# Kernel optimization log

Hardware: AMD Instinct MI355X
Metric: run time of the kernel (lower is better)

The kernel has to match this reference:

```python
import jax, jax.numpy as jnp
import numpy as np

AUDIO_DIM = 1280
FR = 0.15   # freq_mask_ratio
TR = 0.2    # time_mask_ratio
NT = 2      # num_t
NF = 2      # num_f


def setup_inputs() -> dict:
    key = jax.random.key(0)
    k = jax.random.split(key, 6)
    B, T, D = 32, 2048, 1536
    X = jax.random.normal(k[0], (B, T, D), dtype=jnp.float32)
    lengths = jax.random.randint(k[1], (B,), 0, 2048).astype(jnp.int64)
    u_t = jax.random.uniform(k[2], (NT, B), dtype=jnp.float32)
    u_t0 = jax.random.uniform(k[3], (NT, B), dtype=jnp.float32)
    u_f = jax.random.uniform(k[4], (NF, B), dtype=jnp.float32)
    u_f0 = jax.random.uniform(k[5], (NF, B), dtype=jnp.float32)
    return {"X": X, "lengths": lengths, "u_t": u_t, "u_t0": u_t0,
            "u_f": u_f, "u_f0": u_f0}


def reference(X, lengths, u_t, u_t0, u_f, u_f0):
    B, T, D = X.shape
    A = AUDIO_DIM
    V = X[..., : D - A]          # video part, untouched
    Aud = X[..., D - A :]        # audio part, gets masked

    # ---- time masking (per sample, NT spans) ----
    len_i = lengths.astype(jnp.int32)                      # [B]
    max_t = jnp.floor(len_i.astype(jnp.float32) * TR)      # int(Ti*tr), [B]
    # t ~ randint(0, max_t+1): floor(u*(max_t+1))
    t = jnp.floor(u_t * (max_t[None, :] + 1.0)).astype(jnp.int32)   # [NT,B]
    rem = len_i[None, :] - t                                        # Ti - t
    # t0 = 0 if Ti-t<=0 else randint(0, Ti-t+1)
    t0 = jnp.where(rem <= 0, 0,
                   jnp.floor(u_t0 * (rem.astype(jnp.float32) + 1.0)).astype(jnp.int32))
    tt = jnp.arange(T, dtype=jnp.int32)[None, None, :]              # [1,1,T]
    tmask = jnp.any((tt >= t0[:, :, None]) & (tt < (t0 + t)[:, :, None]), axis=0)  # [B,T]

    # ---- frequency masking (per sample, NF spans) ----
    max_f = int(A * FR)
    f = jnp.floor(u_f * (max_f + 1.0)).astype(jnp.int32)            # [NF,B]
    f0_max = jnp.clip(A - f, 0, None)
    f0 = jnp.floor(u_f0 * (f0_max.astype(jnp.float32) + 1.0)).astype(jnp.int32)
    ff = jnp.arange(A, dtype=jnp.int32)[None, None, :]              # [1,1,A]
    fmask = jnp.any((ff >= f0[:, :, None]) & (ff < (f0 + f)[:, :, None]), axis=0)  # [B,A]

    keep = jnp.logical_not(tmask[:, :, None] | fmask[:, None, :]).astype(X.dtype)  # [B,T,A]
    return jnp.concatenate([V, Aud * keep], axis=-1)
```

## Files before the change

### kernel.cpp

```cpp
#include <hip/hip_runtime.h>

#define AUDIO_DIM_ 1280
#define B_ 32
#define T_ 2048
#define D_ 1536
#define V_ (D_ - AUDIO_DIM_)

__global__ void precompute_bounds(const int* __restrict__ lengths,
                                  const float* __restrict__ u_t,
                                  const float* __restrict__ u_t0,
                                  const float* __restrict__ u_f,
                                  const float* __restrict__ u_f0,
                                  int* __restrict__ bounds) {
    int b = threadIdx.x;
    if (b >= B_) return;
    int len = lengths[b];
    float max_t = floorf((float)len * 0.2f);
    int o[8];
    #pragma unroll
    for (int j = 0; j < 2; ++j) {
        int t   = (int)floorf(u_t[j * B_ + b] * (max_t + 1.0f));
        int rem = len - t;
        int t0  = (rem <= 0) ? 0 : (int)floorf(u_t0[j * B_ + b] * ((float)rem + 1.0f));
        o[2 * j]     = t0;
        o[2 * j + 1] = t0 + t;
    }
    #pragma unroll
    for (int j = 0; j < 2; ++j) {
        int f     = (int)floorf(u_f[j * B_ + b] * 193.0f);
        int f0max = AUDIO_DIM_ - f;
        if (f0max < 0) f0max = 0;
        int f0    = (int)floorf(u_f0[j * B_ + b] * ((float)f0max + 1.0f));
        o[4 + 2 * j] = f0;
        o[5 + 2 * j] = f0 + f;
    }
    int4* dst = (int4*)(bounds + b * 8);
    dst[0] = make_int4(o[0], o[1], o[2], o[3]);
    dst[1] = make_int4(o[4], o[5], o[6], o[7]);
}

__device__ __forceinline__ bool in_iv(int v, int lo, int hi) {
    return (v >= lo) && (v < hi);
}

__global__ __launch_bounds__(256) void specaug_kernel(const float4* __restrict__ X,
                                                      float4* __restrict__ out,
                                                      const int4* __restrict__ bounds) {
    constexpr int ND4  = D_ / 4;
    constexpr int NV4  = V_ / 4;
    constexpr int NTD4 = T_ * ND4;
    constexpr int N4   = B_ * NTD4;

    int stride = gridDim.x * blockDim.x;
    for (int idx = blockIdx.x * blockDim.x + threadIdx.x; idx < N4; idx += stride) {
        int b  = idx / NTD4;
        int r  = idx - b * NTD4;
        int t  = r / ND4;
        int d4 = r - t * ND4;

        float4 x = X[idx];

        if (d4 >= NV4) {
            int4 tb = bounds[2 * b];
            bool tm = in_iv(t, tb.x, tb.y) || in_iv(t, tb.z, tb.w);
            if (tm) {
                x = make_float4(0.f, 0.f, 0.f, 0.f);
            } else {
                int4 fb = bounds[2 * b + 1];
                int ff = (d4 - NV4) * 4;
                if (in_iv(ff + 0, fb.x, fb.y) || in_iv(ff + 0, fb.z, fb.w)) x.x = 0.f;
                if (in_iv(ff + 1, fb.x, fb.y) || in_iv(ff + 1, fb.z, fb.w)) x.y = 0.f;
                if (in_iv(ff + 2, fb.x, fb.y) || in_iv(ff + 2, fb.z, fb.w)) x.z = 0.f;
                if (in_iv(ff + 3, fb.x, fb.y) || in_iv(ff + 3, fb.z, fb.w)) x.w = 0.f;
            }
        }
        out[idx] = x;
    }
}

extern "C" void kernel_launch(void* const* d_in, const int* in_sizes, int n_in,
                              void* d_out, int out_size, void* d_ws, size_t ws_size,
                              hipStream_t stream) {
    const float* X       = (const float*)d_in[0];
    const int*   lengths = (const int*)  d_in[1];
    const float* u_t     = (const float*)d_in[2];
    const float* u_t0    = (const float*)d_in[3];
    const float* u_f     = (const float*)d_in[4];
    const float* u_f0    = (const float*)d_in[5];
    float*       out     = (float*)d_out;
    int*         bounds  = (int*)d_ws;

    precompute_bounds<<<1, 64, 0, stream>>>(lengths, u_t, u_t0, u_f, u_f0, bounds);

    specaug_kernel<<<12288, 256, 0, stream>>>((const float4*)X, (float4*)out,
                                              (const int4*)bounds);
}
```

Before: 643.0 us.

## Fuse bounds computation into a row-tiled kernel with nontemporal access and masked-row skipping

Drops the separate bounds-precompute launch; each block now derives its sample's time and frequency spans directly from the inputs. The grid becomes 2D (row tile × batch) with 384 threads covering one row of float4s, which removes the per-element div/mod of the grid-stride loop. The frequency mask is built once per thread as a float4 multiplier. Loads for time-masked audio rows are skipped, and loads and stores are nontemporal. Every block redundantly reads the small per-sample inputs. Multiplying by the mask differs from the reference only for non-finite inputs (NaN or Inf times 0 gives NaN, not 0), which random normal data never produces.

```diff
diff --git a/kernel.cpp b/kernel.cpp
--- a/kernel.cpp
+++ b/kernel.cpp
@@ -5,93 +5,95 @@
 #define T_ 2048
 #define D_ 1536
 #define V_ (D_ - AUDIO_DIM_)
+#define ND4_ (D_ / 4)
+#define NV4_ (V_ / 4)
+#define ROWS_ 8
 
-__global__ void precompute_bounds(const int* __restrict__ lengths,
-                                  const float* __restrict__ u_t,
-                                  const float* __restrict__ u_t0,
-                                  const float* __restrict__ u_f,
-                                  const float* __restrict__ u_f0,
-                                  int* __restrict__ bounds) {
-    int b = threadIdx.x;
-    if (b >= B_) return;
-    int len = lengths[b];
-    float max_t = floorf((float)len * 0.2f);
-    int o[8];
-    #pragma unroll
-    for (int j = 0; j < 2; ++j) {
-        int t   = (int)floorf(u_t[j * B_ + b] * (max_t + 1.0f));
-        int rem = len - t;
-        int t0  = (rem <= 0) ? 0 : (int)floorf(u_t0[j * B_ + b] * ((float)rem + 1.0f));
-        o[2 * j]     = t0;
-        o[2 * j + 1] = t0 + t;
-    }
-    #pragma unroll
-    for (int j = 0; j < 2; ++j) {
-        int f     = (int)floorf(u_f[j * B_ + b] * 193.0f);
-        int f0max = AUDIO_DIM_ - f;
-        if (f0max < 0) f0max = 0;
-        int f0    = (int)floorf(u_f0[j * B_ + b] * ((float)f0max + 1.0f));
-        o[4 + 2 * j] = f0;
-        o[5 + 2 * j] = f0 + f;
-    }
-    int4* dst = (int4*)(bounds + b * 8);
-    dst[0] = make_int4(o[0], o[1], o[2], o[3]);
-    dst[1] = make_int4(o[4], o[5], o[6], o[7]);
-}
+typedef float f4 __attribute__((ext_vector_type(4)));
 
 __device__ __forceinline__ bool in_iv(int v, int lo, int hi) {
     return (v >= lo) && (v < hi);
 }
 
-__global__ __launch_bounds__(256) void specaug_kernel(const float4* __restrict__ X,
-                                                      float4* __restrict__ out,
-                                                      const int4* __restrict__ bounds) {
-    constexpr int ND4  = D_ / 4;
-    constexpr int NV4  = V_ / 4;
-    constexpr int NTD4 = T_ * ND4;
-    constexpr int N4   = B_ * NTD4;
+__global__ __launch_bounds__(384) void specaug_kernel(
+    const f4* __restrict__ X, f4* __restrict__ out,
+    const int*   __restrict__ lengths,
+    const float* __restrict__ u_t,  const float* __restrict__ u_t0,
+    const float* __restrict__ u_f,  const float* __restrict__ u_f0)
+{
+    const int b   = blockIdx.y;
+    const int tb0 = blockIdx.x * ROWS_;
+    const int tid = threadIdx.x;
 
-    int stride = gridDim.x * blockDim.x;
-    for (int idx = blockIdx.x * blockDim.x + threadIdx.x; idx < N4; idx += stride) {
-        int b  = idx / NTD4;
-        int r  = idx - b * NTD4;
-        int t  = r / ND4;
-        int d4 = r - t * ND4;
+    const int   len   = lengths[b];
+    const float max_t = floorf((float)len * 0.2f);
 
-        float4 x = X[idx];
+    int t0a, tea, t0b, teb;
+    {
+        int t   = (int)floorf(u_t[b] * (max_t + 1.0f));
+        int rem = len - t;
+        int t0  = (rem <= 0) ? 0 : (int)floorf(u_t0[b] * ((float)rem + 1.0f));
+        t0a = t0; tea = t0 + t;
 
-        if (d4 >= NV4) {
-            int4 tb = bounds[2 * b];
-            bool tm = in_iv(t, tb.x, tb.y) || in_iv(t, tb.z, tb.w);
-            if (tm) {
-                x = make_float4(0.f, 0.f, 0.f, 0.f);
-            } else {
-                int4 fb = bounds[2 * b + 1];
-                int ff = (d4 - NV4) * 4;
-                if (in_iv(ff + 0, fb.x, fb.y) || in_iv(ff + 0, fb.z, fb.w)) x.x = 0.f;
-                if (in_iv(ff + 1, fb.x, fb.y) || in_iv(ff + 1, fb.z, fb.w)) x.y = 0.f;
-                if (in_iv(ff + 2, fb.x, fb.y) || in_iv(ff + 2, fb.z, fb.w)) x.z = 0.f;
-                if (in_iv(ff + 3, fb.x, fb.y) || in_iv(ff + 3, fb.z, fb.w)) x.w = 0.f;
-            }
+        t   = (int)floorf(u_t[B_ + b] * (max_t + 1.0f));
+        rem = len - t;
+        t0  = (rem <= 0) ? 0 : (int)floorf(u_t0[B_ + b] * ((float)rem + 1.0f));
+        t0b = t0; teb = t0 + t;
+    }
+
+    int f0a, fea, f0b, feb;
+    {
+        int f     = (int)floorf(u_f[b] * 193.0f);
+        int f0max = AUDIO_DIM_ - f; if (f0max < 0) f0max = 0;
+        int f0    = (int)floorf(u_f0[b] * ((float)f0max + 1.0f));
+        f0a = f0; fea = f0 + f;
+
+        f     = (int)floorf(u_f[B_ + b] * 193.0f);
+        f0max = AUDIO_DIM_ - f; if (f0max < 0) f0max = 0;
+        f0    = (int)floorf(u_f0[B_ + b] * ((float)f0max + 1.0f));
+        f0b = f0; feb = f0 + f;
+    }
+
+    const bool isV = (tid < NV4_);
+    float m0 = 1.f, m1 = 1.f, m2 = 1.f, m3 = 1.f;
+    if (!isV) {
+        const int ff = (tid - NV4_) * 4;
+        m0 = (in_iv(ff + 0, f0a, fea) || in_iv(ff + 0, f0b, feb)) ? 0.f : 1.f;
+        m1 = (in_iv(ff + 1, f0a, fea) || in_iv(ff + 1, f0b, feb)) ? 0.f : 1.f;
+        m2 = (in_iv(ff + 2, f0a, fea) || in_iv(ff + 2, f0b, feb)) ? 0.f : 1.f;
+        m3 = (in_iv(ff + 3, f0a, fea) || in_iv(ff + 3, f0b, feb)) ? 0.f : 1.f;
+    }
+    const f4 m = {m0, m1, m2, m3};
+
+    const int base = (b * T_ + tb0) * ND4_ + tid;
+    #pragma unroll
+    for (int r = 0; r < ROWS_; ++r) {
+        const int  t   = tb0 + r;
+        const bool tm  = in_iv(t, t0a, tea) || in_iv(t, t0b, teb);
+        const int  idx = base + r * ND4_;
+
+        f4 x = {0.f, 0.f, 0.f, 0.f};
+        if (isV) {
+            x = __builtin_nontemporal_load(X + idx);
+        } else if (!tm) {
+            x = __builtin_nontemporal_load(X + idx) * m;
         }
-        out[idx] = x;
+        __builtin_nontemporal_store(x, out + idx);
     }
 }
 
 extern "C" void kernel_launch(void* const* d_in, const int* in_sizes, int n_in,
                               void* d_out, int out_size, void* d_ws, size_t ws_size,
                               hipStream_t stream) {
-    const float* X       = (const float*)d_in[0];
+    const f4*    X       = (const f4*)   d_in[0];
     const int*   lengths = (const int*)  d_in[1];
     const float* u_t     = (const float*)d_in[2];
     const float* u_t0    = (const float*)d_in[3];
     const float* u_f     = (const float*)d_in[4];
     const float* u_f0    = (const float*)d_in[5];
-    float*       out     = (float*)d_out;
-    int*         bounds  = (int*)d_ws;
+    f4*          out     = (f4*)d_out;
 
-    precompute_bounds<<<1, 64, 0, stream>>>(lengths, u_t, u_t0, u_f, u_f0, bounds);
-
-    specaug_kernel<<<12288, 256, 0, stream>>>((const float4*)X, (float4*)out,
-                                              (const int4*)bounds);
+    dim3 grid(T_ / ROWS_, B_);
+    specaug_kernel<<<grid, 384, 0, stream>>>(X, out, lengths,
+                                             u_t, u_t0, u_f, u_f0);
 }
```

Measured after the change: 629.4 us. 2.1% less time.
